# Kernel tuning notes

Hardware: AMD Instinct MI355X
Metric: run time of the kernel (lower is better)

The kernel has to match this reference:

```python
import jax, jax.numpy as jnp
import numpy as np

B, T, D, S = 4, 8192, 512, 16

def setup_inputs() -> dict:
    key = jax.random.key(0)
    k1, k2, k3, k4, k5 = jax.random.split(key, 5)
    x = jax.random.normal(k1, (B, T, D), dtype=jnp.float32)
    # splat parameters as in __init__: centers ~ 0.02*randn, log_scales = 0
    centers = jax.random.normal(k2, (S, D), dtype=jnp.float32) * 0.02
    log_scales = jnp.zeros((S,), dtype=jnp.float32)
    # xavier-uniform linear weights (gain = 1/(1+layer_idx*0.1) = 1.0 for layer 0)
    limit = float(np.sqrt(6.0 / (D + D)))
    Wv = jax.random.uniform(k3, (D, D), minval=-limit, maxval=limit, dtype=jnp.float32)
    Wo = jax.random.uniform(k4, (D, D), minval=-limit, maxval=limit, dtype=jnp.float32)
    return {"x": x, "centers": centers, "log_scales": log_scales, "Wv": Wv, "Wo": Wo}

def reference(x, centers, log_scales, Wv, Wo):
    # scales clamped as in EnhancedAdaptiveSplat.get_scale
    scales = jnp.clip(jnp.exp(log_scales), 0.1, 2.0)           # [S]
    v = jnp.einsum('btd,ed->bte', x, Wv)                       # value projection [B,T,D]
    # squared distance token<->splat via expansion (no [B,T,S,D] intermediate)
    x2 = jnp.sum(x * x, axis=-1, keepdims=True)                # [B,T,1]
    c2 = jnp.sum(centers * centers, axis=-1)                   # [S]
    xc = jnp.einsum('btd,sd->bts', x, centers)                 # [B,T,S]
    d2 = x2 + c2 - 2.0 * xc                                    # [B,T,S]
    logits = -0.5 * d2 / (scales * scales)                     # gaussian kernel log-weights
    attn = jax.nn.softmax(logits, axis=-1)                     # normalize over splats [B,T,S]
    # tokens -> splats aggregation, then splats -> tokens distribution
    splat_states = jnp.einsum('bts,btd->bsd', attn, v)         # [B,S,D]
    out = jnp.einsum('bts,bsd->btd', attn, splat_states)       # [B,T,D]
    return jnp.einsum('btd,ed->bte', out, Wo)                  # output projection
```

## Files before the change

kernel.cpp:

```cpp
#include <hip/hip_runtime.h>
#include <hip/hip_bf16.h>
#include <math.h>

#define B_ 4
#define T_ 8192
#define D_ 512
#define S_ 16

__device__ __forceinline__ float reduce_scatter16(float vals[S_], int lane) {
  {
    const int bit = (lane >> 5) & 1;
#pragma unroll
    for (int i = 0; i < 8; ++i) {
      float send = bit ? vals[i] : vals[i + 8];
      float keep = bit ? vals[i + 8] : vals[i];
      vals[i] = keep + __shfl_xor(send, 32, 64);
    }
  }
  {
    const int bit = (lane >> 4) & 1;
#pragma unroll
    for (int i = 0; i < 4; ++i) {
      float send = bit ? vals[i] : vals[i + 4];
      float keep = bit ? vals[i + 4] : vals[i];
      vals[i] = keep + __shfl_xor(send, 16, 64);
    }
  }
  {
    const int bit = (lane >> 3) & 1;
#pragma unroll
    for (int i = 0; i < 2; ++i) {
      float send = bit ? vals[i] : vals[i + 2];
      float keep = bit ? vals[i + 2] : vals[i];
      vals[i] = keep + __shfl_xor(send, 8, 64);
    }
  }
  {
    const int bit = (lane >> 2) & 1;
    float send = bit ? vals[0] : vals[1];
    float keep = bit ? vals[1] : vals[0];
    float v = keep + __shfl_xor(send, 4, 64);
    v += __shfl_xor(v, 2, 64);
    v += __shfl_xor(v, 1, 64);
    return v;
  }
}

__device__ __forceinline__ float dot4(float4 a, float4 b) {
  return a.x * b.x + a.y * b.y + a.z * b.z + a.w * b.w;
}

__global__ __launch_bounds__(256) void attn_k(const float* __restrict__ x,
                                              const float* __restrict__ centers,
                                              const float* __restrict__ log_scales,
                                              float* __restrict__ attn) {
  const int lane = threadIdx.x & 63;
  const int wid = (blockIdx.x << 2) + (threadIdx.x >> 6);
  const int nw = gridDim.x << 2;
  const int myS = (lane >> 2) & 15;

  float4 c_reg[S_][2];
#pragma unroll
  for (int s = 0; s < S_; ++s)
#pragma unroll
    for (int j = 0; j < 2; ++j)
      c_reg[s][j] = *(const float4*)(centers + s * D_ + (j << 8) + (lane << 2));

  float c2;
  {
    float vals[S_];
#pragma unroll
    for (int s = 0; s < S_; ++s)
      vals[s] = dot4(c_reg[s][0], c_reg[s][0]) + dot4(c_reg[s][1], c_reg[s][1]);
    c2 = reduce_scatter16(vals, lane);
  }
  const float sc = fminf(fmaxf(__expf(log_scales[myS]), 0.1f), 2.0f);
  const float inv2 = 0.5f / (sc * sc);

  const int total = B_ * T_;
  for (int t = wid; t < total; t += nw) {
    const float* xr = x + (size_t)t * D_;
    float4 xv0 = *(const float4*)(xr + (lane << 2));
    float4 xv1 = *(const float4*)(xr + 256 + (lane << 2));
    float x2p = dot4(xv0, xv0) + dot4(xv1, xv1);

    float vals[S_];
#pragma unroll
    for (int s = 0; s < S_; ++s)
      vals[s] = x2p - 2.f * (dot4(xv0, c_reg[s][0]) + dot4(xv1, c_reg[s][1]));

    float v = reduce_scatter16(vals, lane);
    float logit = -(v + c2) * inv2;

    float m = logit;
    m = fmaxf(m, __shfl_xor(m, 4, 64));
    m = fmaxf(m, __shfl_xor(m, 8, 64));
    m = fmaxf(m, __shfl_xor(m, 16, 64));
    m = fmaxf(m, __shfl_xor(m, 32, 64));
    float e = __expf(logit - m);
    float ssum = e;
    ssum += __shfl_xor(ssum, 4, 64);
    ssum += __shfl_xor(ssum, 8, 64);
    ssum += __shfl_xor(ssum, 16, 64);
    ssum += __shfl_xor(ssum, 32, 64);
    if ((lane & 3) == 0) attn[(size_t)t * S_ + myS] = e / ssum;
  }
}

#define K2_TOK 128
__global__ __launch_bounds__(512) void ts_k(const float* __restrict__ x,
                                            const float* __restrict__ attn,
                                            float* __restrict__ ts) {
  const int chunks = T_ / K2_TOK;
  const int b = blockIdx.x / chunks;
  const int t0 = (blockIdx.x % chunks) * K2_TOK;
  const int d = threadIdx.x;

  float acc[S_];
#pragma unroll
  for (int s = 0; s < S_; ++s) acc[s] = 0.f;

  const float* xb = x + ((size_t)b * T_ + t0) * D_ + d;
  const float4* ab = (const float4*)(attn + ((size_t)b * T_ + t0) * S_);

#pragma unroll 4
  for (int t = 0; t < K2_TOK; ++t) {
    float xv = xb[(size_t)t * D_];
    float4 a0 = ab[t * 4 + 0], a1 = ab[t * 4 + 1];
    float4 a2 = ab[t * 4 + 2], a3 = ab[t * 4 + 3];
    acc[0]  += a0.x * xv; acc[1]  += a0.y * xv; acc[2]  += a0.z * xv; acc[3]  += a0.w * xv;
    acc[4]  += a1.x * xv; acc[5]  += a1.y * xv; acc[6]  += a1.z * xv; acc[7]  += a1.w * xv;
    acc[8]  += a2.x * xv; acc[9]  += a2.y * xv; acc[10] += a2.z * xv; acc[11] += a2.w * xv;
    acc[12] += a3.x * xv; acc[13] += a3.y * xv; acc[14] += a3.z * xv; acc[15] += a3.w * xv;
  }

  float* tb = ts + (size_t)b * S_ * D_ + d;
#pragma unroll
  for (int s = 0; s < S_; ++s) atomicAdd(tb + s * D_, acc[s]);
}

__global__ __launch_bounds__(256) void proj_k(const float* __restrict__ in,
                                              const float* __restrict__ W,
                                              float* __restrict__ out) {
  const int gid = blockIdx.x * 256 + threadIdx.x;
  const int e = gid & 511;
  const int rk = gid >> 9;
  const int r = rk >> 2;
  const int kc = rk & 3;
  const float4* w4 = (const float4*)(W + (size_t)e * D_ + kc * 128);
  const float4* i4 = (const float4*)(in + (size_t)r * D_ + kc * 128);
  float acc = 0.f;
#pragma unroll
  for (int k = 0; k < 32; ++k) acc += dot4(w4[k], i4[k]);
  atomicAdd(out + (size_t)r * D_ + e, acc);
}

#define K4_TOK 128
__global__ __launch_bounds__(256) void out_k(const float* __restrict__ attn,
                                             const float* __restrict__ ss_o,
                                             float* __restrict__ out) {
  const int chunks = T_ / K4_TOK;
  const int b = blockIdx.x / chunks;
  const int t0 = (blockIdx.x % chunks) * K4_TOK;
  const int w = threadIdx.x >> 6;
  const int lane = threadIdx.x & 63;
  const int e0 = (w << 7) + (lane << 1);

  float2 ssf[S_];
  const float* sb = ss_o + (size_t)b * S_ * D_;
#pragma unroll
  for (int s = 0; s < S_; ++s) ssf[s] = *(const float2*)(sb + s * D_ + e0);

  const float4* ab = (const float4*)(attn + ((size_t)b * T_ + t0) * S_);
  float* ob = out + ((size_t)b * T_ + t0) * D_ + e0;

#pragma unroll 2
  for (int t = 0; t < K4_TOK; ++t) {
    float4 a0 = ab[t * 4 + 0], a1 = ab[t * 4 + 1];
    float4 a2 = ab[t * 4 + 2], a3 = ab[t * 4 + 3];
    float av[S_] = {a0.x, a0.y, a0.z, a0.w, a1.x, a1.y, a1.z, a1.w,
                    a2.x, a2.y, a2.z, a2.w, a3.x, a3.y, a3.z, a3.w};
    float2 acc = make_float2(0.f, 0.f);
#pragma unroll
    for (int s = 0; s < S_; ++s) {
      acc.x += av[s] * ssf[s].x;
      acc.y += av[s] * ssf[s].y;
    }
    *(float2*)(ob + (size_t)t * D_) = acc;
  }
}

extern "C" void kernel_launch(void* const* d_in, const int* in_sizes, int n_in,
                              void* d_out, int out_size, void* d_ws, size_t ws_size,
                              hipStream_t stream) {
  const float* x          = (const float*)d_in[0];
  const float* centers    = (const float*)d_in[1];
  const float* log_scales = (const float*)d_in[2];
  const float* Wv         = (const float*)d_in[3];
  const float* Wo         = (const float*)d_in[4];
  float* out = (float*)d_out;

  float* attn = (float*)d_ws;
  float* ts   = attn + (size_t)B_ * T_ * S_;
  float* tmp  = ts + (size_t)B_ * S_ * D_;
  float* ss_o = tmp + (size_t)B_ * S_ * D_;

  hipMemsetAsync(ts, 0, (size_t)3 * B_ * S_ * D_ * sizeof(float), stream);

  attn_k<<<2048, 256, 0, stream>>>(x, centers, log_scales, attn);
  ts_k<<<B_ * (T_ / K2_TOK), 512, 0, stream>>>(x, attn, ts);
  proj_k<<<512, 256, 0, stream>>>(ts, Wv, tmp);
  proj_k<<<512, 256, 0, stream>>>(tmp, Wo, ss_o);
  out_k<<<B_ * (T_ / K4_TOK), 256, 0, stream>>>(attn, ss_o, out);
}
```

Measured before the change: 202.7 us.

## Fold memset into attn kernel, pair tokens, and drop atomics in projection

The separate memset launch is removed and the ts buffer is zeroed inside attn_k instead. attn_k now processes two tokens per wave iteration for more ILP, with a launch bound of 2. proj_k reduces its four k-chunks through shared memory rather than global atomics, which makes the output writes deterministic. Unroll factors and the out_k token chunk size are also adjusted. Zeroing ts inside attn_k is safe because ts_k runs only after attn_k completes, though the extra register pressure from pairing tokens could limit occupancy.

```diff
diff --git a/kernel.cpp b/kernel.cpp
--- a/kernel.cpp
+++ b/kernel.cpp
@@ -50,10 +50,15 @@
   return a.x * b.x + a.y * b.y + a.z * b.z + a.w * b.w;
 }
 
-__global__ __launch_bounds__(256) void attn_k(const float* __restrict__ x,
-                                              const float* __restrict__ centers,
-                                              const float* __restrict__ log_scales,
-                                              float* __restrict__ attn) {
+__global__ __launch_bounds__(256, 2) void attn_k(const float* __restrict__ x,
+                                                 const float* __restrict__ centers,
+                                                 const float* __restrict__ log_scales,
+                                                 float* __restrict__ attn,
+                                                 float* __restrict__ ts) {
+  if (blockIdx.x < 64) {
+    *(float2*)(ts + blockIdx.x * 512 + threadIdx.x * 2) = make_float2(0.f, 0.f);
+  }
+
   const int lane = threadIdx.x & 63;
   const int wid = (blockIdx.x << 2) + (threadIdx.x >> 6);
   const int nw = gridDim.x << 2;
@@ -77,33 +82,45 @@
   const float sc = fminf(fmaxf(__expf(log_scales[myS]), 0.1f), 2.0f);
   const float inv2 = 0.5f / (sc * sc);
 
-  const int total = B_ * T_;
-  for (int t = wid; t < total; t += nw) {
-    const float* xr = x + (size_t)t * D_;
-    float4 xv0 = *(const float4*)(xr + (lane << 2));
-    float4 xv1 = *(const float4*)(xr + 256 + (lane << 2));
-    float x2p = dot4(xv0, xv0) + dot4(xv1, xv1);
-
-    float vals[S_];
-#pragma unroll
-    for (int s = 0; s < S_; ++s)
-      vals[s] = x2p - 2.f * (dot4(xv0, c_reg[s][0]) + dot4(xv1, c_reg[s][1]));
-
-    float v = reduce_scatter16(vals, lane);
-    float logit = -(v + c2) * inv2;
-
-    float m = logit;
-    m = fmaxf(m, __shfl_xor(m, 4, 64));
-    m = fmaxf(m, __shfl_xor(m, 8, 64));
-    m = fmaxf(m, __shfl_xor(m, 16, 64));
-    m = fmaxf(m, __shfl_xor(m, 32, 64));
-    float e = __expf(logit - m);
-    float ssum = e;
-    ssum += __shfl_xor(ssum, 4, 64);
-    ssum += __shfl_xor(ssum, 8, 64);
-    ssum += __shfl_xor(ssum, 16, 64);
-    ssum += __shfl_xor(ssum, 32, 64);
-    if ((lane & 3) == 0) attn[(size_t)t * S_ + myS] = e / ssum;
+  const int npairs = (B_ * T_) / 2;
+  for (int tp = wid; tp < npairs; tp += nw) {
+    const int t0 = tp << 1;
+    const float* xr = x + (size_t)t0 * D_;
+    float4 a0 = *(const float4*)(xr + (lane << 2));
+    float4 a1 = *(const float4*)(xr + 256 + (lane << 2));
+    float4 b0 = *(const float4*)(xr + 512 + (lane << 2));
+    float4 b1 = *(const float4*)(xr + 768 + (lane << 2));
+
+    float x2a = dot4(a0, a0) + dot4(a1, a1);
+    float x2b = dot4(b0, b0) + dot4(b1, b1);
+
+    float va[S_], vb[S_];
+#pragma unroll
+    for (int s = 0; s < S_; ++s) {
+      va[s] = x2a - 2.f * (dot4(a0, c_reg[s][0]) + dot4(a1, c_reg[s][1]));
+      vb[s] = x2b - 2.f * (dot4(b0, c_reg[s][0]) + dot4(b1, c_reg[s][1]));
+    }
+
+    float ra = reduce_scatter16(va, lane);
+    float rb = reduce_scatter16(vb, lane);
+    float la = -(ra + c2) * inv2;
+    float lb = -(rb + c2) * inv2;
+
+    float ma = la, mb = lb;
+    ma = fmaxf(ma, __shfl_xor(ma, 4, 64));  mb = fmaxf(mb, __shfl_xor(mb, 4, 64));
+    ma = fmaxf(ma, __shfl_xor(ma, 8, 64));  mb = fmaxf(mb, __shfl_xor(mb, 8, 64));
+    ma = fmaxf(ma, __shfl_xor(ma, 16, 64)); mb = fmaxf(mb, __shfl_xor(mb, 16, 64));
+    ma = fmaxf(ma, __shfl_xor(ma, 32, 64)); mb = fmaxf(mb, __shfl_xor(mb, 32, 64));
+    float ea = __expf(la - ma), eb = __expf(lb - mb);
+    float sa = ea, sb = eb;
+    sa += __shfl_xor(sa, 4, 64);  sb += __shfl_xor(sb, 4, 64);
+    sa += __shfl_xor(sa, 8, 64);  sb += __shfl_xor(sb, 8, 64);
+    sa += __shfl_xor(sa, 16, 64); sb += __shfl_xor(sb, 16, 64);
+    sa += __shfl_xor(sa, 32, 64); sb += __shfl_xor(sb, 32, 64);
+    if ((lane & 3) == 0) {
+      attn[(size_t)t0 * S_ + myS] = ea / sa;
+      attn[(size_t)(t0 + 1) * S_ + myS] = eb / sb;
+    }
   }
 }
 
@@ -123,7 +140,7 @@
   const float* xb = x + ((size_t)b * T_ + t0) * D_ + d;
   const float4* ab = (const float4*)(attn + ((size_t)b * T_ + t0) * S_);
 
-#pragma unroll 4
+#pragma unroll 16
   for (int t = 0; t < K2_TOK; ++t) {
     float xv = xb[(size_t)t * D_];
     float4 a0 = ab[t * 4 + 0], a1 = ab[t * 4 + 1];
@@ -142,20 +159,26 @@
 __global__ __launch_bounds__(256) void proj_k(const float* __restrict__ in,
                                               const float* __restrict__ W,
                                               float* __restrict__ out) {
-  const int gid = blockIdx.x * 256 + threadIdx.x;
-  const int e = gid & 511;
-  const int rk = gid >> 9;
-  const int r = rk >> 2;
-  const int kc = rk & 3;
+  __shared__ float red[4][64];
+  const int r = blockIdx.x >> 3;
+  const int eb = blockIdx.x & 7;
+  const int el = threadIdx.x & 63;
+  const int kc = threadIdx.x >> 6;
+  const int e = (eb << 6) + el;
+
   const float4* w4 = (const float4*)(W + (size_t)e * D_ + kc * 128);
   const float4* i4 = (const float4*)(in + (size_t)r * D_ + kc * 128);
   float acc = 0.f;
 #pragma unroll
   for (int k = 0; k < 32; ++k) acc += dot4(w4[k], i4[k]);
-  atomicAdd(out + (size_t)r * D_ + e, acc);
-}
-
-#define K4_TOK 128
+
+  red[kc][el] = acc;
+  __syncthreads();
+  if (kc == 0)
+    out[(size_t)r * D_ + e] = red[0][el] + red[1][el] + red[2][el] + red[3][el];
+}
+
+#define K4_TOK 64
 __global__ __launch_bounds__(256) void out_k(const float* __restrict__ attn,
                                              const float* __restrict__ ss_o,
                                              float* __restrict__ out) {
@@ -174,7 +197,7 @@
   const float4* ab = (const float4*)(attn + ((size_t)b * T_ + t0) * S_);
   float* ob = out + ((size_t)b * T_ + t0) * D_ + e0;
 
-#pragma unroll 2
+#pragma unroll 4
   for (int t = 0; t < K4_TOK; ++t) {
     float4 a0 = ab[t * 4 + 0], a1 = ab[t * 4 + 1];
     float4 a2 = ab[t * 4 + 2], a3 = ab[t * 4 + 3];
@@ -205,9 +228,7 @@
   float* tmp  = ts + (size_t)B_ * S_ * D_;
   float* ss_o = tmp + (size_t)B_ * S_ * D_;
 
-  hipMemsetAsync(ts, 0, (size_t)3 * B_ * S_ * D_ * sizeof(float), stream);
-
-  attn_k<<<2048, 256, 0, stream>>>(x, centers, log_scales, attn);
+  attn_k<<<2048, 256, 0, stream>>>(x, centers, log_scales, attn, ts);
   ts_k<<<B_ * (T_ / K2_TOK), 512, 0, stream>>>(x, attn, ts);
   proj_k<<<512, 256, 0, stream>>>(ts, Wv, tmp);
   proj_k<<<512, 256, 0, stream>>>(tmp, Wo, ss_o);
```

Measured after the change: 194.0 us. -4.3%, faster.
